# Kernel optimization log

Measured on AMD Instinct MI355X. Metric: run time of the kernel, lower is better.

Reference implementation:

```python
import jax, jax.numpy as jnp
import numpy as np

W_MAE, W_GRAD, W_TV, W_BG, W_MSE = 1.0, 0.1, 0.002, 0.15, 1.0
EPS = 1e-8


def setup_inputs() -> dict:
    key = jax.random.key(0)
    k1, k2, k3 = jax.random.split(key, 3)
    B, C, D, H, W = 2, 3, 128, 128, 128
    pred = jax.random.normal(k1, (B, C, D, H, W), dtype=jnp.float32)
    target = jax.random.normal(k2, (B, C, D, H, W), dtype=jnp.float32)
    # binary foreground mask, broadcast over channels
    mask = (jax.random.uniform(k3, (B, 1, D, H, W)) > 0.5).astype(jnp.float32)
    return {"pred": pred, "target": target, "mask": mask}


def _grad3(x):
    dx = x[:, :, 1:, :, :] - x[:, :, :-1, :, :]
    dy = x[:, :, :, 1:, :] - x[:, :, :, :-1, :]
    dz = x[:, :, :, :, 1:] - x[:, :, :, :, :-1]
    return dx, dy, dz


def reference(pred, target, mask):
    C = pred.shape[1]

    def masked_mean(x, m):
        return (x * m).sum() / (m.sum() * C + EPS)

    pred_in = pred * mask
    tgt_in = target * mask
    diff = pred_in - tgt_in

    l_mae = masked_mean(jnp.abs(diff), mask)

    px, py, pz = _grad3(pred_in)
    tx, ty, tz = _grad3(tgt_in)
    mx = jnp.minimum(mask[:, :, 1:, :, :], mask[:, :, :-1, :, :])
    my = jnp.minimum(mask[:, :, :, 1:, :], mask[:, :, :, :-1, :])
    mz = jnp.minimum(mask[:, :, :, :, 1:], mask[:, :, :, :, :-1])

    l_grad = (masked_mean(jnp.abs(px - tx), mx)
              + masked_mean(jnp.abs(py - ty), my)
              + masked_mean(jnp.abs(pz - tz), mz))
    l_tv = (masked_mean(jnp.abs(px), mx)
            + masked_mean(jnp.abs(py), my)
            + masked_mean(jnp.abs(pz), mz))

    inv = 1.0 - mask
    l_bg = (jnp.abs(pred) * inv).sum() / (inv.sum() * C + EPS)

    l_mse = masked_mean(diff ** 2, mask)

    return (W_MAE * l_mae + W_GRAD * l_grad + W_TV * l_tv
            + W_BG * l_bg + W_MSE * l_mse)
```

## Files before the change

### kernel.cpp

```cpp
#include <hip/hip_runtime.h>

#define NACC 13
#define NPAD 16
#define NBLOCKS 4096
#define NROWS 16384
#define NMID 64

__device__ __forceinline__ float4 ld4(const float* p) {
    return *reinterpret_cast<const float4*>(p);
}

__global__ __launch_bounds__(256, 3) void loss_main(
    const float* __restrict__ pred, const float* __restrict__ target,
    const float* __restrict__ mask, float* __restrict__ partials)
{
    float acc[NACC];
#pragma unroll
    for (int k = 0; k < NACC; ++k) acc[k] = 0.f;

    const int g  = blockIdx.x * 256 + threadIdx.x;
    const int w4 = g & 31;
    const int h  = (g >> 5) & 127;
    const int d  = (g >> 12) & 127;
    const int b  = g >> 19;
    const int w  = w4 << 2;
    const int mb  = b * 2097152 + d * 16384 + h * 128 + w;
    const int pb0 = b * 6291456 + d * 16384 + h * 128 + w;

    const float wv = (w4 < 31) ? 1.f : 0.f;
    const float hv = (h < 127) ? 1.f : 0.f;
    const float dv = (d < 127) ? 1.f : 0.f;
    const int oh = (h < 127) ? 128   : 0;
    const int od = (d < 127) ? 16384 : 0;

    const float4 m0 = ld4(mask + mb);
    const float4 mh = ld4(mask + mb + oh);
    const float4 md = ld4(mask + mb + od);
    float4 P0[3], T0[3], PH[3], TH[3], PD[3], TD[3];
#pragma unroll
    for (int c = 0; c < 3; ++c) {
        const int pb = pb0 + c * 2097152;
        P0[c] = ld4(pred + pb);
        T0[c] = ld4(target + pb);
        PD[c] = ld4(pred + pb + od);
        TD[c] = ld4(target + pb + od);
        PH[c] = ld4(pred + pb + oh);
        TH[c] = ld4(target + pb + oh);
    }
    __builtin_amdgcn_sched_barrier(0);

    const float m4w = __shfl_down(m0.x, 1, 64);

    const float mz0 = fminf(m0.x, m0.y), mz1 = fminf(m0.y, m0.z),
                mz2 = fminf(m0.z, m0.w), mz3 = fminf(m0.w, m4w) * wv;
    const float my0 = fminf(m0.x, mh.x) * hv, my1 = fminf(m0.y, mh.y) * hv,
                my2 = fminf(m0.z, mh.z) * hv, my3 = fminf(m0.w, mh.w) * hv;
    const float mx0 = fminf(m0.x, md.x) * dv, mx1 = fminf(m0.y, md.y) * dv,
                mx2 = fminf(m0.z, md.z) * dv, mx3 = fminf(m0.w, md.w) * dv;

    acc[0] = m0.x + m0.y + m0.z + m0.w;
    acc[1] = mx0 + mx1 + mx2 + mx3;
    acc[2] = my0 + my1 + my2 + my3;
    acc[3] = mz0 + mz1 + mz2 + mz3;

#pragma unroll
    for (int c = 0; c < 3; ++c) {
        const float4 p0 = P0[c], t0 = T0[c];
        const float4 ph = PH[c], th = TH[c];
        const float4 pd = PD[c], td = TD[c];
        const float  p4 = __shfl_down(p0.x, 1, 64);
        const float  t4 = __shfl_down(t0.x, 1, 64);

        const float e0x = p0.x - t0.x, e0y = p0.y - t0.y,
                    e0z = p0.z - t0.z, e0w = p0.w - t0.w;
        const float e4  = p4 - t4;

        acc[4] += fabsf(e0x)*m0.x + fabsf(e0y)*m0.y
                + fabsf(e0z)*m0.z + fabsf(e0w)*m0.w;
        acc[5] += e0x*e0x*m0.x + e0y*e0y*m0.y
                + e0z*e0z*m0.z + e0w*e0w*m0.w;
        acc[6] += fabsf(p0.x)*(1.f-m0.x) + fabsf(p0.y)*(1.f-m0.y)
                + fabsf(p0.z)*(1.f-m0.z) + fabsf(p0.w)*(1.f-m0.w);

        acc[9]  += fabsf(e0y-e0x)*mz0 + fabsf(e0z-e0y)*mz1
                 + fabsf(e0w-e0z)*mz2 + fabsf(e4 -e0w)*mz3;
        acc[12] += fabsf(p0.y-p0.x)*mz0 + fabsf(p0.z-p0.y)*mz1
                 + fabsf(p0.w-p0.z)*mz2 + fabsf(p4  -p0.w)*mz3;

        acc[8]  += fabsf((ph.x-th.x)-e0x)*my0 + fabsf((ph.y-th.y)-e0y)*my1
                 + fabsf((ph.z-th.z)-e0z)*my2 + fabsf((ph.w-th.w)-e0w)*my3;
        acc[11] += fabsf(ph.x-p0.x)*my0 + fabsf(ph.y-p0.y)*my1
                 + fabsf(ph.z-p0.z)*my2 + fabsf(ph.w-p0.w)*my3;

        acc[7]  += fabsf((pd.x-td.x)-e0x)*mx0 + fabsf((pd.y-td.y)-e0y)*mx1
                 + fabsf((pd.z-td.z)-e0z)*mx2 + fabsf((pd.w-td.w)-e0w)*mx3;
        acc[10] += fabsf(pd.x-p0.x)*mx0 + fabsf(pd.y-p0.y)*mx1
                 + fabsf(pd.z-p0.z)*mx2 + fabsf(pd.w-p0.w)*mx3;
    }

    const int lane = threadIdx.x & 63;
    const int wave = threadIdx.x >> 6;
    float mine = 0.f;
#pragma unroll
    for (int k = 0; k < NACC; ++k) {
        float v = acc[k];
        for (int o = 32; o > 0; o >>= 1) v += __shfl_down(v, o, 64);
        const float tot = __shfl(v, 0, 64);
        if (lane == k) mine = tot;
    }
    if (lane < NPAD)
        partials[(blockIdx.x * 4 + wave) * NPAD + lane] = mine;
}

__global__ __launch_bounds__(256) void loss_mid(
    const float* __restrict__ partials, float* __restrict__ mid)
{
    const int r = blockIdx.x * 256 + threadIdx.x;
    const float* row = partials + r * NPAD;
    const float4 r0 = ld4(row);     const float4 r1 = ld4(row + 4);
    const float4 r2 = ld4(row + 8); const float4 r3 = ld4(row + 12);
    float acc[NPAD] = {r0.x, r0.y, r0.z, r0.w, r1.x, r1.y, r1.z, r1.w,
                       r2.x, r2.y, r2.z, r2.w, r3.x, r3.y, r3.z, r3.w};

    const int lane = threadIdx.x & 63;
    const int wave = threadIdx.x >> 6;
    __shared__ float red[4][NPAD];
#pragma unroll
    for (int k = 0; k < NPAD; ++k) {
        float v = acc[k];
        for (int o = 32; o > 0; o >>= 1) v += __shfl_down(v, o, 64);
        if (lane == 0) red[wave][k] = v;
    }
    __syncthreads();
    if (threadIdx.x < NPAD) {
        const int k = threadIdx.x;
        mid[blockIdx.x * NPAD + k] =
            red[0][k] + red[1][k] + red[2][k] + red[3][k];
    }
}

__global__ __launch_bounds__(64) void loss_final(
    const float* __restrict__ mid, float* __restrict__ out)
{
    const int lane = threadIdx.x;
    float acc[NPAD];
    {
        const float* row = mid + lane * NPAD;
        const float4 r0 = ld4(row);     const float4 r1 = ld4(row + 4);
        const float4 r2 = ld4(row + 8); const float4 r3 = ld4(row + 12);
        acc[0] = r0.x;  acc[1] = r0.y;  acc[2] = r0.z;  acc[3] = r0.w;
        acc[4] = r1.x;  acc[5] = r1.y;  acc[6] = r1.z;  acc[7] = r1.w;
        acc[8] = r2.x;  acc[9] = r2.y;  acc[10] = r2.z; acc[11] = r2.w;
        acc[12] = r3.x; acc[13] = r3.y; acc[14] = r3.z; acc[15] = r3.w;
    }
#pragma unroll
    for (int k = 0; k < NACC; ++k) {
        for (int o = 32; o > 0; o >>= 1) acc[k] += __shfl_down(acc[k], o, 64);
    }
    if (lane == 0) {
        const float EPS = 1e-8f;
        const float M = acc[0], Mx = acc[1], My = acc[2], Mz = acc[3];
        float loss = (acc[4] + acc[5]) / (3.f * M + EPS);
        loss += 0.1f   * (acc[7] / (3.f*Mx + EPS) + acc[8] / (3.f*My + EPS)
                        + acc[9] / (3.f*Mz + EPS));
        loss += 0.002f * (acc[10] / (3.f*Mx + EPS) + acc[11] / (3.f*My + EPS)
                        + acc[12] / (3.f*Mz + EPS));
        const float inv = 4194304.f - M;
        loss += 0.15f * acc[6] / (3.f * inv + EPS);
        out[0] = loss;
    }
}

extern "C" void kernel_launch(void* const* d_in, const int* in_sizes, int n_in,
                              void* d_out, int out_size, void* d_ws, size_t ws_size,
                              hipStream_t stream) {
    const float* pred   = (const float*)d_in[0];
    const float* target = (const float*)d_in[1];
    const float* mask   = (const float*)d_in[2];
    float* out      = (float*)d_out;
    float* partials = (float*)d_ws;
    float* mid      = partials + NROWS * NPAD;

    loss_main<<<NBLOCKS, 256, 0, stream>>>(pred, target, mask, partials);
    loss_mid<<<NMID, 256, 0, stream>>>(partials, mid);
    loss_final<<<1, 64, 0, stream>>>(mid, out);
}
```

Before: 140.9 us.

## Process two depth slices per thread to reuse neighbour loads

```diff
diff --git a/kernel.cpp b/kernel.cpp
--- a/kernel.cpp
+++ b/kernel.cpp
@@ -2,15 +2,15 @@
 
 #define NACC 13
 #define NPAD 16
-#define NBLOCKS 4096
-#define NROWS 16384
-#define NMID 64
+#define NBLOCKS 2048
+#define NROWS 8192
+#define NMID 32
 
 __device__ __forceinline__ float4 ld4(const float* p) {
     return *reinterpret_cast<const float4*>(p);
 }
 
-__global__ __launch_bounds__(256, 3) void loss_main(
+__global__ __launch_bounds__(256, 2) void loss_main(
     const float* __restrict__ pred, const float* __restrict__ target,
     const float* __restrict__ mask, float* __restrict__ partials)
 {
@@ -21,81 +21,113 @@
     const int g  = blockIdx.x * 256 + threadIdx.x;
     const int w4 = g & 31;
     const int h  = (g >> 5) & 127;
-    const int d  = (g >> 12) & 127;
-    const int b  = g >> 19;
+    const int dp = (g >> 12) & 63;
+    const int b  = g >> 18;
     const int w  = w4 << 2;
-    const int mb  = b * 2097152 + d * 16384 + h * 128 + w;
-    const int pb0 = b * 6291456 + d * 16384 + h * 128 + w;
+    const int d0 = dp << 1;
 
     const float wv = (w4 < 31) ? 1.f : 0.f;
     const float hv = (h < 127) ? 1.f : 0.f;
-    const float dv = (d < 127) ? 1.f : 0.f;
-    const int oh = (h < 127) ? 128   : 0;
-    const int od = (d < 127) ? 16384 : 0;
-
-    const float4 m0 = ld4(mask + mb);
-    const float4 mh = ld4(mask + mb + oh);
-    const float4 md = ld4(mask + mb + od);
-    float4 P0[3], T0[3], PH[3], TH[3], PD[3], TD[3];
+    const float dv = (dp < 63) ? 1.f : 0.f;
+    const int oh  = (h < 127) ? 128 : 0;
+    const int od2 = (dp < 63) ? 32768 : 0;
+
+    const int mb  = b * 2097152 + d0 * 16384 + h * 128 + w;
+    const int pb0 = b * 6291456 + d0 * 16384 + h * 128 + w;
+
+    const float4 a0  = ld4(mask + mb);
+    const float4 a1  = ld4(mask + mb + 16384);
+    const float4 a2  = ld4(mask + mb + od2);
+    const float4 ah0 = ld4(mask + mb + oh);
+    const float4 ah1 = ld4(mask + mb + 16384 + oh);
+    float4 P0[3], T0[3], P1[3], T1[3], PH0[3], TH0[3],
+           PH1[3], TH1[3], P2[3], T2[3];
 #pragma unroll
     for (int c = 0; c < 3; ++c) {
         const int pb = pb0 + c * 2097152;
-        P0[c] = ld4(pred + pb);
-        T0[c] = ld4(target + pb);
-        PD[c] = ld4(pred + pb + od);
-        TD[c] = ld4(target + pb + od);
-        PH[c] = ld4(pred + pb + oh);
-        TH[c] = ld4(target + pb + oh);
+        P0[c]  = ld4(pred + pb);             T0[c]  = ld4(target + pb);
+        P1[c]  = ld4(pred + pb + 16384);     T1[c]  = ld4(target + pb + 16384);
+        PH0[c] = ld4(pred + pb + oh);        TH0[c] = ld4(target + pb + oh);
+        PH1[c] = ld4(pred + pb + 16384+oh);  TH1[c] = ld4(target + pb + 16384+oh);
+        P2[c]  = ld4(pred + pb + od2);       T2[c]  = ld4(target + pb + od2);
     }
     __builtin_amdgcn_sched_barrier(0);
 
-    const float m4w = __shfl_down(m0.x, 1, 64);
-
-    const float mz0 = fminf(m0.x, m0.y), mz1 = fminf(m0.y, m0.z),
-                mz2 = fminf(m0.z, m0.w), mz3 = fminf(m0.w, m4w) * wv;
-    const float my0 = fminf(m0.x, mh.x) * hv, my1 = fminf(m0.y, mh.y) * hv,
-                my2 = fminf(m0.z, mh.z) * hv, my3 = fminf(m0.w, mh.w) * hv;
-    const float mx0 = fminf(m0.x, md.x) * dv, mx1 = fminf(m0.y, md.y) * dv,
-                mx2 = fminf(m0.z, md.z) * dv, mx3 = fminf(m0.w, md.w) * dv;
-
-    acc[0] = m0.x + m0.y + m0.z + m0.w;
-    acc[1] = mx0 + mx1 + mx2 + mx3;
-    acc[2] = my0 + my1 + my2 + my3;
-    acc[3] = mz0 + mz1 + mz2 + mz3;
+    const float m4w0 = __shfl_down(a0.x, 1, 64);
+    const float m4w1 = __shfl_down(a1.x, 1, 64);
+
+    const float z00=fminf(a0.x,a0.y), z01=fminf(a0.y,a0.z),
+                z02=fminf(a0.z,a0.w), z03=fminf(a0.w,m4w0)*wv;
+    const float z10=fminf(a1.x,a1.y), z11=fminf(a1.y,a1.z),
+                z12=fminf(a1.z,a1.w), z13=fminf(a1.w,m4w1)*wv;
+    const float y00=fminf(a0.x,ah0.x)*hv, y01=fminf(a0.y,ah0.y)*hv,
+                y02=fminf(a0.z,ah0.z)*hv, y03=fminf(a0.w,ah0.w)*hv;
+    const float y10=fminf(a1.x,ah1.x)*hv, y11=fminf(a1.y,ah1.y)*hv,
+                y12=fminf(a1.z,ah1.z)*hv, y13=fminf(a1.w,ah1.w)*hv;
+    const float x00=fminf(a0.x,a1.x), x01=fminf(a0.y,a1.y),
+                x02=fminf(a0.z,a1.z), x03=fminf(a0.w,a1.w);
+    const float x10=fminf(a1.x,a2.x)*dv, x11=fminf(a1.y,a2.y)*dv,
+                x12=fminf(a1.z,a2.z)*dv, x13=fminf(a1.w,a2.w)*dv;
+
+    acc[0] = a0.x+a0.y+a0.z+a0.w + a1.x+a1.y+a1.z+a1.w;
+    acc[1] = x00+x01+x02+x03 + x10+x11+x12+x13;
+    acc[2] = y00+y01+y02+y03 + y10+y11+y12+y13;
+    acc[3] = z00+z01+z02+z03 + z10+z11+z12+z13;
 
 #pragma unroll
     for (int c = 0; c < 3; ++c) {
-        const float4 p0 = P0[c], t0 = T0[c];
-        const float4 ph = PH[c], th = TH[c];
-        const float4 pd = PD[c], td = TD[c];
-        const float  p4 = __shfl_down(p0.x, 1, 64);
-        const float  t4 = __shfl_down(t0.x, 1, 64);
-
-        const float e0x = p0.x - t0.x, e0y = p0.y - t0.y,
-                    e0z = p0.z - t0.z, e0w = p0.w - t0.w;
-        const float e4  = p4 - t4;
-
-        acc[4] += fabsf(e0x)*m0.x + fabsf(e0y)*m0.y
-                + fabsf(e0z)*m0.z + fabsf(e0w)*m0.w;
-        acc[5] += e0x*e0x*m0.x + e0y*e0y*m0.y
-                + e0z*e0z*m0.z + e0w*e0w*m0.w;
-        acc[6] += fabsf(p0.x)*(1.f-m0.x) + fabsf(p0.y)*(1.f-m0.y)
-                + fabsf(p0.z)*(1.f-m0.z) + fabsf(p0.w)*(1.f-m0.w);
-
-        acc[9]  += fabsf(e0y-e0x)*mz0 + fabsf(e0z-e0y)*mz1
-                 + fabsf(e0w-e0z)*mz2 + fabsf(e4 -e0w)*mz3;
-        acc[12] += fabsf(p0.y-p0.x)*mz0 + fabsf(p0.z-p0.y)*mz1
-                 + fabsf(p0.w-p0.z)*mz2 + fabsf(p4  -p0.w)*mz3;
-
-        acc[8]  += fabsf((ph.x-th.x)-e0x)*my0 + fabsf((ph.y-th.y)-e0y)*my1
-                 + fabsf((ph.z-th.z)-e0z)*my2 + fabsf((ph.w-th.w)-e0w)*my3;
-        acc[11] += fabsf(ph.x-p0.x)*my0 + fabsf(ph.y-p0.y)*my1
-                 + fabsf(ph.z-p0.z)*my2 + fabsf(ph.w-p0.w)*my3;
-
-        acc[7]  += fabsf((pd.x-td.x)-e0x)*mx0 + fabsf((pd.y-td.y)-e0y)*mx1
-                 + fabsf((pd.z-td.z)-e0z)*mx2 + fabsf((pd.w-td.w)-e0w)*mx3;
-        acc[10] += fabsf(pd.x-p0.x)*mx0 + fabsf(pd.y-p0.y)*mx1
-                 + fabsf(pd.z-p0.z)*mx2 + fabsf(pd.w-p0.w)*mx3;
+        const float4 p0 = P0[c],  t0 = T0[c];
+        const float4 p1 = P1[c],  t1 = T1[c];
+        const float4 h0 = PH0[c], g0 = TH0[c];
+        const float4 h1 = PH1[c], g1 = TH1[c];
+        const float4 p2 = P2[c],  t2 = T2[c];
+        const float p4_0 = __shfl_down(p0.x, 1, 64);
+        const float t4_0 = __shfl_down(t0.x, 1, 64);
+        const float p4_1 = __shfl_down(p1.x, 1, 64);
+        const float t4_1 = __shfl_down(t1.x, 1, 64);
+
+        const float e0x=p0.x-t0.x, e0y=p0.y-t0.y, e0z=p0.z-t0.z, e0w=p0.w-t0.w;
+        const float e1x=p1.x-t1.x, e1y=p1.y-t1.y, e1z=p1.z-t1.z, e1w=p1.w-t1.w;
+        const float e4_0 = p4_0 - t4_0, e4_1 = p4_1 - t4_1;
+        const float e2x=p2.x-t2.x, e2y=p2.y-t2.y, e2z=p2.z-t2.z, e2w=p2.w-t2.w;
+
+        acc[4] += fabsf(e0x)*a0.x + fabsf(e0y)*a0.y
+                + fabsf(e0z)*a0.z + fabsf(e0w)*a0.w
+                + fabsf(e1x)*a1.x + fabsf(e1y)*a1.y
+                + fabsf(e1z)*a1.z + fabsf(e1w)*a1.w;
+        acc[5] += e0x*e0x*a0.x + e0y*e0y*a0.y + e0z*e0z*a0.z + e0w*e0w*a0.w
+                + e1x*e1x*a1.x + e1y*e1y*a1.y + e1z*e1z*a1.z + e1w*e1w*a1.w;
+        acc[6] += fabsf(p0.x)*(1.f-a0.x) + fabsf(p0.y)*(1.f-a0.y)
+                + fabsf(p0.z)*(1.f-a0.z) + fabsf(p0.w)*(1.f-a0.w)
+                + fabsf(p1.x)*(1.f-a1.x) + fabsf(p1.y)*(1.f-a1.y)
+                + fabsf(p1.z)*(1.f-a1.z) + fabsf(p1.w)*(1.f-a1.w);
+
+        acc[9]  += fabsf(e0y-e0x)*z00 + fabsf(e0z-e0y)*z01
+                 + fabsf(e0w-e0z)*z02 + fabsf(e4_0-e0w)*z03
+                 + fabsf(e1y-e1x)*z10 + fabsf(e1z-e1y)*z11
+                 + fabsf(e1w-e1z)*z12 + fabsf(e4_1-e1w)*z13;
+        acc[12] += fabsf(p0.y-p0.x)*z00 + fabsf(p0.z-p0.y)*z01
+                 + fabsf(p0.w-p0.z)*z02 + fabsf(p4_0-p0.w)*z03
+                 + fabsf(p1.y-p1.x)*z10 + fabsf(p1.z-p1.y)*z11
+                 + fabsf(p1.w-p1.z)*z12 + fabsf(p4_1-p1.w)*z13;
+
+        acc[8]  += fabsf((h0.x-g0.x)-e0x)*y00 + fabsf((h0.y-g0.y)-e0y)*y01
+                 + fabsf((h0.z-g0.z)-e0z)*y02 + fabsf((h0.w-g0.w)-e0w)*y03
+                 + fabsf((h1.x-g1.x)-e1x)*y10 + fabsf((h1.y-g1.y)-e1y)*y11
+                 + fabsf((h1.z-g1.z)-e1z)*y12 + fabsf((h1.w-g1.w)-e1w)*y13;
+        acc[11] += fabsf(h0.x-p0.x)*y00 + fabsf(h0.y-p0.y)*y01
+                 + fabsf(h0.z-p0.z)*y02 + fabsf(h0.w-p0.w)*y03
+                 + fabsf(h1.x-p1.x)*y10 + fabsf(h1.y-p1.y)*y11
+                 + fabsf(h1.z-p1.z)*y12 + fabsf(h1.w-p1.w)*y13;
+
+        acc[7]  += fabsf(e1x-e0x)*x00 + fabsf(e1y-e0y)*x01
+                 + fabsf(e1z-e0z)*x02 + fabsf(e1w-e0w)*x03
+                 + fabsf(e2x-e1x)*x10 + fabsf(e2y-e1y)*x11
+                 + fabsf(e2z-e1z)*x12 + fabsf(e2w-e1w)*x13;
+        acc[10] += fabsf(p1.x-p0.x)*x00 + fabsf(p1.y-p0.y)*x01
+                 + fabsf(p1.z-p0.z)*x02 + fabsf(p1.w-p0.w)*x03
+                 + fabsf(p2.x-p1.x)*x10 + fabsf(p2.y-p1.y)*x11
+                 + fabsf(p2.z-p1.z)*x12 + fabsf(p2.w-p1.w)*x13;
     }
 
     const int lane = threadIdx.x & 63;
@@ -144,7 +176,7 @@
 {
     const int lane = threadIdx.x;
     float acc[NPAD];
-    {
+    if (lane < NMID) {
         const float* row = mid + lane * NPAD;
         const float4 r0 = ld4(row);     const float4 r1 = ld4(row + 4);
         const float4 r2 = ld4(row + 8); const float4 r3 = ld4(row + 12);
@@ -152,6 +184,9 @@
         acc[4] = r1.x;  acc[5] = r1.y;  acc[6] = r1.z;  acc[7] = r1.w;
         acc[8] = r2.x;  acc[9] = r2.y;  acc[10] = r2.z; acc[11] = r2.w;
         acc[12] = r3.x; acc[13] = r3.y; acc[14] = r3.z; acc[15] = r3.w;
+    } else {
+#pragma unroll
+        for (int k = 0; k < NPAD; ++k) acc[k] = 0.f;
     }
 #pragma unroll
     for (int k = 0; k < NACC; ++k) {
```

New measurement: 141.3 us. No clear change (+0.3%).

## Process four voxel slabs per thread with double-buffered register loads

Applied to the files above, without the earlier changes.

```diff
diff --git a/kernel.cpp b/kernel.cpp
--- a/kernel.cpp
+++ b/kernel.cpp
@@ -2,53 +2,39 @@
 
 #define NACC 13
 #define NPAD 16
-#define NBLOCKS 4096
-#define NROWS 16384
-#define NMID 64
+#define NBLOCKS 1024
+#define NROWS 4096
+#define NMID 16
 
 __device__ __forceinline__ float4 ld4(const float* p) {
     return *reinterpret_cast<const float4*>(p);
 }
 
-__global__ __launch_bounds__(256, 3) void loss_main(
+struct Regs {
+    float4 m0, mh, md;
+    float4 P0[3], T0[3], PH[3], TH[3], PD[3], TD[3];
+};
+
+__device__ __forceinline__ void issue_loads(
     const float* __restrict__ pred, const float* __restrict__ target,
-    const float* __restrict__ mask, float* __restrict__ partials)
-{
-    float acc[NACC];
-#pragma unroll
-    for (int k = 0; k < NACC; ++k) acc[k] = 0.f;
-
-    const int g  = blockIdx.x * 256 + threadIdx.x;
-    const int w4 = g & 31;
-    const int h  = (g >> 5) & 127;
-    const int d  = (g >> 12) & 127;
-    const int b  = g >> 19;
-    const int w  = w4 << 2;
-    const int mb  = b * 2097152 + d * 16384 + h * 128 + w;
-    const int pb0 = b * 6291456 + d * 16384 + h * 128 + w;
-
-    const float wv = (w4 < 31) ? 1.f : 0.f;
-    const float hv = (h < 127) ? 1.f : 0.f;
-    const float dv = (d < 127) ? 1.f : 0.f;
-    const int oh = (h < 127) ? 128   : 0;
-    const int od = (d < 127) ? 16384 : 0;
-
-    const float4 m0 = ld4(mask + mb);
-    const float4 mh = ld4(mask + mb + oh);
-    const float4 md = ld4(mask + mb + od);
-    float4 P0[3], T0[3], PH[3], TH[3], PD[3], TD[3];
+    const float* __restrict__ mask, int mb, int pb0, int oh, int od, Regs& r)
+{
+    r.m0 = ld4(mask + mb);
+    r.mh = ld4(mask + mb + oh);
+    r.md = ld4(mask + mb + od);
 #pragma unroll
     for (int c = 0; c < 3; ++c) {
         const int pb = pb0 + c * 2097152;
-        P0[c] = ld4(pred + pb);
-        T0[c] = ld4(target + pb);
-        PD[c] = ld4(pred + pb + od);
-        TD[c] = ld4(target + pb + od);
-        PH[c] = ld4(pred + pb + oh);
-        TH[c] = ld4(target + pb + oh);
-    }
-    __builtin_amdgcn_sched_barrier(0);
-
+        r.P0[c] = ld4(pred + pb);       r.T0[c] = ld4(target + pb);
+        r.PD[c] = ld4(pred + pb + od);  r.TD[c] = ld4(target + pb + od);
+        r.PH[c] = ld4(pred + pb + oh);  r.TH[c] = ld4(target + pb + oh);
+    }
+}
+
+__device__ __forceinline__ void consume(
+    const Regs& r, float wv, float hv, float dv, float* acc)
+{
+    const float4 m0 = r.m0, mh = r.mh, md = r.md;
     const float m4w = __shfl_down(m0.x, 1, 64);
 
     const float mz0 = fminf(m0.x, m0.y), mz1 = fminf(m0.y, m0.z),
@@ -58,16 +44,16 @@
     const float mx0 = fminf(m0.x, md.x) * dv, mx1 = fminf(m0.y, md.y) * dv,
                 mx2 = fminf(m0.z, md.z) * dv, mx3 = fminf(m0.w, md.w) * dv;
 
-    acc[0] = m0.x + m0.y + m0.z + m0.w;
-    acc[1] = mx0 + mx1 + mx2 + mx3;
-    acc[2] = my0 + my1 + my2 + my3;
-    acc[3] = mz0 + mz1 + mz2 + mz3;
+    acc[0] += m0.x + m0.y + m0.z + m0.w;
+    acc[1] += mx0 + mx1 + mx2 + mx3;
+    acc[2] += my0 + my1 + my2 + my3;
+    acc[3] += mz0 + mz1 + mz2 + mz3;
 
 #pragma unroll
     for (int c = 0; c < 3; ++c) {
-        const float4 p0 = P0[c], t0 = T0[c];
-        const float4 ph = PH[c], th = TH[c];
-        const float4 pd = PD[c], td = TD[c];
+        const float4 p0 = r.P0[c], t0 = r.T0[c];
+        const float4 ph = r.PH[c], th = r.TH[c];
+        const float4 pd = r.PD[c], td = r.TD[c];
         const float  p4 = __shfl_down(p0.x, 1, 64);
         const float  t4 = __shfl_down(t0.x, 1, 64);
 
@@ -97,6 +83,52 @@
         acc[10] += fabsf(pd.x-p0.x)*mx0 + fabsf(pd.y-p0.y)*mx1
                  + fabsf(pd.z-p0.z)*mx2 + fabsf(pd.w-p0.w)*mx3;
     }
+}
+
+__global__ __launch_bounds__(256, 2) void loss_main(
+    const float* __restrict__ pred, const float* __restrict__ target,
+    const float* __restrict__ mask, float* __restrict__ partials)
+{
+    float acc[NACC];
+#pragma unroll
+    for (int k = 0; k < NACC; ++k) acc[k] = 0.f;
+
+    const int base = blockIdx.x * 256 + threadIdx.x;
+    const int w4   = base & 31;
+    const int h    = (base >> 5) & 127;
+    const int dlow = (base >> 12) & 63;
+    const int w    = w4 << 2;
+
+    const float wv = (w4 < 31) ? 1.f : 0.f;
+    const float hv = (h < 127) ? 1.f : 0.f;
+    const int   oh = (h < 127) ? 128 : 0;
+    const float dv_e = 1.f;
+    const int   od_e = 16384;
+    const float dv_o = (dlow < 63) ? 1.f : 0.f;
+    const int   od_o = (dlow < 63) ? 16384 : 0;
+
+    const int mb00 = dlow * 16384 + h * 128 + w;
+    const int mb0 = mb00,            pb0 = mb00;
+    const int mb1 = mb00 + 1048576,  pb1 = mb00 + 1048576;
+    const int mb2 = mb00 + 2097152,  pb2 = mb00 + 6291456;
+    const int mb3 = mb00 + 3145728,  pb3 = mb00 + 7340032;
+
+    Regs A, B;
+    issue_loads(pred, target, mask, mb0, pb0, oh, od_e, A);
+    __builtin_amdgcn_sched_barrier(0);
+    issue_loads(pred, target, mask, mb1, pb1, oh, od_o, B);
+    __builtin_amdgcn_sched_barrier(0);
+    consume(A, wv, hv, dv_e, acc);
+    __builtin_amdgcn_sched_barrier(0);
+    issue_loads(pred, target, mask, mb2, pb2, oh, od_e, A);
+    __builtin_amdgcn_sched_barrier(0);
+    consume(B, wv, hv, dv_o, acc);
+    __builtin_amdgcn_sched_barrier(0);
+    issue_loads(pred, target, mask, mb3, pb3, oh, od_o, B);
+    __builtin_amdgcn_sched_barrier(0);
+    consume(A, wv, hv, dv_e, acc);
+    __builtin_amdgcn_sched_barrier(0);
+    consume(B, wv, hv, dv_o, acc);
 
     const int lane = threadIdx.x & 63;
     const int wave = threadIdx.x >> 6;
@@ -144,7 +176,7 @@
 {
     const int lane = threadIdx.x;
     float acc[NPAD];
-    {
+    if (lane < NMID) {
         const float* row = mid + lane * NPAD;
         const float4 r0 = ld4(row);     const float4 r1 = ld4(row + 4);
         const float4 r2 = ld4(row + 8); const float4 r3 = ld4(row + 12);
@@ -152,6 +184,9 @@
         acc[4] = r1.x;  acc[5] = r1.y;  acc[6] = r1.z;  acc[7] = r1.w;
         acc[8] = r2.x;  acc[9] = r2.y;  acc[10] = r2.z; acc[11] = r2.w;
         acc[12] = r3.x; acc[13] = r3.y; acc[14] = r3.z; acc[15] = r3.w;
+    } else {
+#pragma unroll
+        for (int k = 0; k < NPAD; ++k) acc[k] = 0.f;
     }
 #pragma unroll
     for (int k = 0; k < NACC; ++k) {
```

New measurement: 142.0 us. Within noise of the previous version (+0.8%).
